# Optimization experiments

Measured on AMD Instinct MI355X. Metric: run time of the kernel, lower is better.

## Reference

```python
import jax, jax.numpy as jnp
import numpy as np

NUM_EXPERTS = 8
INPUT_SIZE = 2048
OUTPUT_SIZE = 8192
EXPERT_SIZES = np.array([3000, 5000, 4096, 2048, 6000, 4000, 4624, 4000], dtype=np.int64)  # sums to 32768
TOTAL_TOKENS = int(EXPERT_SIZES.sum())


def setup_inputs() -> dict:
    key = jax.random.key(0)
    k_in, k_w = jax.random.split(key)
    inputs = jax.random.normal(k_in, (TOTAL_TOKENS, INPUT_SIZE), dtype=jnp.float32)
    # per-expert Linear weights, torch layout [out, in]
    weights = jax.random.normal(k_w, (NUM_EXPERTS, OUTPUT_SIZE, INPUT_SIZE), dtype=jnp.float32) * 0.02
    expert_size = jnp.asarray(EXPERT_SIZES)
    return {"inputs": inputs, "weights": weights, "expert_size": expert_size}


def reference(inputs, weights, expert_size):
    # Grouped GEMM: split tokens by static per-expert counts, y_i = x_i @ W_i^T, concat.
    sizes = [int(s) for s in np.asarray(expert_size)]
    offsets = np.concatenate([[0], np.cumsum(sizes)])
    outs = []
    for i in range(len(sizes)):
        x_i = inputs[offsets[i]:offsets[i + 1]]  # [n_i, input_size]
        outs.append(jnp.einsum('ti,oi->to', x_i, weights[i]))  # [n_i, output_size]
    return jnp.concatenate(outs, axis=0)  # [total_tokens, output_size]
```

## Files before the change

### kernel.cpp

```cpp
#include <hip/hip_runtime.h>

typedef __bf16 bf16x8 __attribute__((ext_vector_type(8)));
typedef float  f32x4  __attribute__((ext_vector_type(4)));

#define KDIM 2048
#define NDIM 8192
#define MTOT 32768
#define BM 256
#define BN 256
#define BK 64
#define NT 32
#define NMT 131
#define NWG (NMT * 32)

__device__ __forceinline__ void gload_lds16(const void* g, void* l) {
    __builtin_amdgcn_global_load_lds(
        (const __attribute__((address_space(1))) void*)g,
        (__attribute__((address_space(3))) void*)l, 16, 0, 0);
}

__global__ __launch_bounds__(256) void convert_f32_bf16(
    const float* __restrict__ src, __bf16* __restrict__ dst, int n8)
{
    const int stride = gridDim.x * blockDim.x;
    for (int i = blockIdx.x * blockDim.x + threadIdx.x; i < n8; i += stride) {
        const f32x4* p = (const f32x4*)(src + (size_t)i * 8);
        f32x4 a = p[0], b = p[1];
        bf16x8 h;
        #pragma unroll
        for (int j = 0; j < 4; ++j) { h[j] = (__bf16)a[j]; h[4 + j] = (__bf16)b[j]; }
        *(bf16x8*)(dst + (size_t)i * 8) = h;
    }
}

__global__ void __launch_bounds__(512, 2) moe_gemm_4ph(
    const __bf16* __restrict__ A,
    const __bf16* __restrict__ W,
    float* __restrict__ C)
{
    __shared__ __bf16 As[2][BM * BK];
    __shared__ __bf16 Bs[2][BN * BK];

    const int tstart[9] = {0, 12, 32, 48, 56, 80, 96, 115, 131};
    const int offs[9]   = {0, 3000, 8000, 12096, 14144, 20144, 24144, 28768, 32768};

    const int bid = blockIdx.x;
    const int mt = bid >> 5;
    const int nt = bid & 31;

    int e = 0;
    #pragma unroll
    for (int i = 1; i < 8; ++i) e += (mt >= tstart[i]) ? 1 : 0;
    const int row0 = offs[e] + (mt - tstart[e]) * BM;
    int rows = offs[e + 1] - row0;
    if (rows > BM) rows = BM;
    const int col0 = nt * BN;

    const int tid  = threadIdx.x;
    const int lane = tid & 63;
    const int w    = tid >> 6;
    const int wm   = w >> 2;
    const int wn   = w & 3;

    const int lrow = lane >> 3;
    const int csrc = ((lane & 7) ^ lrow) * 8;

    const __bf16 *aX[2], *aY[2], *b0[2], *b1[2];
    int ldsAX[2], ldsAY[2], ldsB0[2], ldsB1[2];
    #pragma unroll
    for (int c = 0; c < 2; ++c) {
        const int q  = w * 2 + c;
        const int tX = q * 8 + (q & 8) * 8;
        const int tY = tX + 64;
        int rX = tX + lrow; rX = (rX < rows) ? rX : 0;
        int rY = tY + lrow; rY = (rY < rows) ? rY : 0;
        aX[c] = A + (size_t)(row0 + rX) * KDIM + csrc;
        aY[c] = A + (size_t)(row0 + rY) * KDIM + csrc;
        b0[c] = W + (size_t)(e * NDIM + col0 + q * 8 + lrow) * KDIM + csrc;
        b1[c] = W + (size_t)(e * NDIM + col0 + 128 + q * 8 + lrow) * KDIM + csrc;
        ldsAX[c] = tX * BK;
        ldsAY[c] = tY * BK;
        ldsB0[c] = (q * 8) * BK;
        ldsB1[c] = (128 + q * 8) * BK;
    }

#define STAGE_AX(p, o) { gload_lds16(aX[0] + (o), &As[p][ldsAX[0]]); \
                         gload_lds16(aX[1] + (o), &As[p][ldsAX[1]]); }
#define STAGE_AY(p, o) { gload_lds16(aY[0] + (o), &As[p][ldsAY[0]]); \
                         gload_lds16(aY[1] + (o), &As[p][ldsAY[1]]); }
#define STAGE_B0(p, o) { gload_lds16(b0[0] + (o), &Bs[p][ldsB0[0]]); \
                         gload_lds16(b0[1] + (o), &Bs[p][ldsB0[1]]); }
#define STAGE_B1(p, o) { gload_lds16(b1[0] + (o), &Bs[p][ldsB1[0]]); \
                         gload_lds16(b1[1] + (o), &Bs[p][ldsB1[1]]); }

    const int frow = lane & 15;
    const int g8   = (lane >> 4) * 8;
    const int swc  = (frow & 7) << 3;
    const int ck0  = g8 ^ swc;
    const int ck1  = (32 + g8) ^ swc;
    const int arow = wm * 128 + frow;
    const int brow = wn * 64 + frow;

    f32x4 acc[8][4];
    #pragma unroll
    for (int m = 0; m < 8; ++m)
        #pragma unroll
        for (int n = 0; n < 4; ++n)
            acc[m][n] = (f32x4){0.f, 0.f, 0.f, 0.f};

    bf16x8 bk0[4], bk1[4];

#define RD_B(p) { _Pragma("unroll") for (int n = 0; n < 4; ++n) { \
        bk0[n] = *(const bf16x8*)&Bs[p][(brow + n * 16) * BK + ck0]; \
        bk1[n] = *(const bf16x8*)&Bs[p][(brow + n * 16) * BK + ck1]; } }

#define MPHASE(p, h, STAGE, DOVM) { \
    bf16x8 av0[4], av1[4]; \
    _Pragma("unroll") for (int mm = 0; mm < 4; ++mm) { \
        av0[mm] = *(const bf16x8*)&As[p][(arow + (4 * (h) + mm) * 16) * BK + ck0]; \
        av1[mm] = *(const bf16x8*)&As[p][(arow + (4 * (h) + mm) * 16) * BK + ck1]; \
    } \
    STAGE; \
    if (DOVM) { asm volatile("s_waitcnt vmcnt(6)" ::: "memory"); } \
    __builtin_amdgcn_s_barrier(); \
    __builtin_amdgcn_s_setprio(1); \
    _Pragma("unroll") for (int mm = 0; mm < 4; ++mm) \
        _Pragma("unroll") for (int n = 0; n < 4; ++n) \
            acc[4 * (h) + mm][n] = __builtin_amdgcn_mfma_f32_16x16x32_bf16( \
                av0[mm], bk0[n], acc[4 * (h) + mm][n], 0, 0, 0); \
    _Pragma("unroll") for (int mm = 0; mm < 4; ++mm) \
        _Pragma("unroll") for (int n = 0; n < 4; ++n) \
            acc[4 * (h) + mm][n] = __builtin_amdgcn_mfma_f32_16x16x32_bf16( \
                av1[mm], bk1[n], acc[4 * (h) + mm][n], 0, 0, 0); \
    __builtin_amdgcn_s_setprio(0); }

    STAGE_AX(0, 0); STAGE_AY(0, 0); STAGE_B0(0, 0); STAGE_B1(0, 0);
    STAGE_B0(1, BK); STAGE_B1(1, BK); STAGE_AX(1, BK);
    asm volatile("s_waitcnt vmcnt(6)" ::: "memory");
    __builtin_amdgcn_s_barrier();

    #pragma unroll 1
    for (int i = 0; i < 16; ++i) {
        const int t1o = (2 * i + 1) * BK;
        int s2 = 2 * i + 2; if (s2 > NT - 1) s2 = NT - 1;
        int s3 = 2 * i + 3; if (s3 > NT - 1) s3 = NT - 1;
        const int s2o = s2 * BK;
        const int s3o = s3 * BK;

        RD_B(0);
        MPHASE(0, 0, { STAGE_AY(1, t1o); }, 0);
        MPHASE(0, 1, { STAGE_B0(0, s2o); STAGE_B1(0, s2o); STAGE_AX(0, s2o); }, 1);

        RD_B(1);
        MPHASE(1, 0, { STAGE_AY(0, s2o); }, 0);
        MPHASE(1, 1, { STAGE_B0(1, s3o); STAGE_B1(1, s3o); STAGE_AX(1, s3o); }, 1);
    }

    const int crow = (lane >> 4) * 4;
    const int ccol = lane & 15;
    #pragma unroll
    for (int m = 0; m < 8; ++m) {
        #pragma unroll
        for (int j2 = 0; j2 < 4; ++j2) {
            const int r = wm * 128 + m * 16 + crow + j2;
            if (r < rows) {
                float* dst = C + (size_t)(row0 + r) * NDIM + col0 + wn * 64 + ccol;
                #pragma unroll
                for (int n = 0; n < 4; ++n)
                    dst[n * 16] = acc[m][n][j2];
            }
        }
    }
#undef STAGE_AX
#undef STAGE_AY
#undef STAGE_B0
#undef STAGE_B1
#undef RD_B
#undef MPHASE
}

__global__ __launch_bounds__(256) void moe_gemm_f32(
    const float* __restrict__ A, const float* __restrict__ W, float* __restrict__ C)
{
    __shared__ __bf16 Asb[128][64];
    __shared__ __bf16 Bsb[128][64];

    const int tstart[9] = {0, 24, 64, 96, 112, 159, 191, 228, 260};
    const int offs[9]   = {0, 3000, 8000, 12096, 14144, 20144, 24144, 28768, 32768};

    const int mt = blockIdx.y;
    int e = 0;
    #pragma unroll
    for (int i = 1; i < 8; ++i) e += (mt >= tstart[i]) ? 1 : 0;
    const int row0 = offs[e] + (mt - tstart[e]) * 128;
    int rows = offs[e + 1] - row0;
    if (rows > 128) rows = 128;
    const int col0 = blockIdx.x * 128;

    const float* __restrict__ Abase = A + (size_t)row0 * KDIM;
    const float* __restrict__ Wbase = W + ((size_t)e * NDIM + (size_t)col0) * KDIM;

    const int tid  = threadIdx.x;
    const int lane = tid & 63;
    const int wid  = tid >> 6;
    const int wr   = (wid >> 1) * 64;
    const int wc   = (wid & 1) * 64;
    const int srow = tid >> 2;
    const int scol = (tid & 3) * 16;

    f32x4 acc[4][4];
    #pragma unroll
    for (int m = 0; m < 4; ++m)
        #pragma unroll
        for (int n = 0; n < 4; ++n)
            acc[m][n] = (f32x4){0.f, 0.f, 0.f, 0.f};
    const f32x4 fzero = (f32x4){0.f, 0.f, 0.f, 0.f};

    for (int k0 = 0; k0 < KDIM; k0 += 64) {
        __syncthreads();
        #pragma unroll
        for (int rr = 0; rr < 2; ++rr) {
            const int r = srow + rr * 64;
            {
                const bool valid = (r < rows);
                const float* pa = Abase + (size_t)r * KDIM + k0 + scol;
                f32x4 v[4];
                #pragma unroll
                for (int i = 0; i < 4; ++i) v[i] = valid ? *(const f32x4*)(pa + 4 * i) : fzero;
                bf16x8 h0, h1;
                #pragma unroll
                for (int i = 0; i < 8; ++i) {
                    h0[i] = (__bf16)v[i >> 2][i & 3];
                    h1[i] = (__bf16)v[2 + (i >> 2)][i & 3];
                }
                *((bf16x8*)&Asb[r][scol]) = h0;
                *((bf16x8*)&Asb[r][scol + 8]) = h1;
            }
            {
                const float* pb = Wbase + (size_t)r * KDIM + k0 + scol;
                f32x4 v[4];
                #pragma unroll
                for (int i = 0; i < 4; ++i) v[i] = *(const f32x4*)(pb + 4 * i);
                bf16x8 h0, h1;
                #pragma unroll
                for (int i = 0; i < 8; ++i) {
                    h0[i] = (__bf16)v[i >> 2][i & 3];
                    h1[i] = (__bf16)v[2 + (i >> 2)][i & 3];
                }
                *((bf16x8*)&Bsb[r][scol]) = h0;
                *((bf16x8*)&Bsb[r][scol + 8]) = h1;
            }
        }
        __syncthreads();
        #pragma unroll
        for (int ks = 0; ks < 2; ++ks) {
            const int kb = ks * 32 + (lane >> 4) * 8;
            bf16x8 af[4], bfr[4];
            #pragma unroll
            for (int m = 0; m < 4; ++m)
                af[m] = *((const bf16x8*)&Asb[wr + m * 16 + (lane & 15)][kb]);
            #pragma unroll
            for (int n = 0; n < 4; ++n)
                bfr[n] = *((const bf16x8*)&Bsb[wc + n * 16 + (lane & 15)][kb]);
            #pragma unroll
            for (int m = 0; m < 4; ++m)
                #pragma unroll
                for (int n = 0; n < 4; ++n)
                    acc[m][n] = __builtin_amdgcn_mfma_f32_16x16x32_bf16(
                        af[m], bfr[n], acc[m][n], 0, 0, 0);
        }
    }

    const int crow = (lane >> 4) * 4;
    const int ccol = lane & 15;
    #pragma unroll
    for (int m = 0; m < 4; ++m) {
        #pragma unroll
        for (int j = 0; j < 4; ++j) {
            const int r = wr + m * 16 + crow + j;
            if (r < rows) {
                float* dst = C + (size_t)(row0 + r) * NDIM + col0 + wc + ccol;
                #pragma unroll
                for (int n = 0; n < 4; ++n)
                    dst[n * 16] = acc[m][n][j];
            }
        }
    }
}

extern "C" void kernel_launch(void* const* d_in, const int* in_sizes, int n_in,
                              void* d_out, int out_size, void* d_ws, size_t ws_size,
                              hipStream_t stream) {
    const float* A = (const float*)d_in[0];
    const float* W = (const float*)d_in[1];
    float* C = (float*)d_out;

    const size_t nA = (size_t)MTOT * KDIM;
    const size_t nW = (size_t)8 * NDIM * KDIM;
    const size_t WS_NEED = (nA + nW) * 2;

    if (ws_size >= WS_NEED) {
        __bf16* Abf = (__bf16*)d_ws;
        __bf16* Wbf = (__bf16*)((char*)d_ws + nA * 2);
        hipLaunchKernelGGL(convert_f32_bf16, dim3(2048), dim3(256), 0, stream,
                           A, Abf, (int)(nA / 8));
        hipLaunchKernelGGL(convert_f32_bf16, dim3(2048), dim3(256), 0, stream,
                           W, Wbf, (int)(nW / 8));
        hipLaunchKernelGGL(moe_gemm_4ph, dim3(NWG), dim3(512), 0, stream,
                           Abf, Wbf, C);
    } else {
        hipLaunchKernelGGL(moe_gemm_f32, dim3(NDIM / 128, 260), dim3(256), 0, stream,
                           A, W, C);
    }
}
```

Before: 1.266 ms.

## Double-buffer LDS-to-register fragments so reads overlap the previous MFMA cluster

Restructures the main loop so each phase issues its global staging and barrier first, then loads the next A/B fragments from LDS into a second register set before running the MFMA cluster on the already-loaded set. sched_barrier fences keep the compiler from interleaving the two. The aim is to hide LDS read latency behind matrix-core work. In exchange it doubles fragment register usage, which risks spills or pressure at the 512-thread, 2-block launch bound. It also changes barrier placement relative to buffer overwrites, which could open hazards.

```diff
diff --git a/kernel.cpp b/kernel.cpp
--- a/kernel.cpp
+++ b/kernel.cpp
@@ -33,7 +33,7 @@
     }
 }
 
-__global__ void __launch_bounds__(512, 2) moe_gemm_4ph(
+__global__ void __launch_bounds__(512, 2) moe_gemm_rdb(
     const __bf16* __restrict__ A,
     const __bf16* __restrict__ W,
     float* __restrict__ C)
@@ -108,36 +108,38 @@
         for (int n = 0; n < 4; ++n)
             acc[m][n] = (f32x4){0.f, 0.f, 0.f, 0.f};
 
-    bf16x8 bk0[4], bk1[4];
-
-#define RD_B(p) { _Pragma("unroll") for (int n = 0; n < 4; ++n) { \
-        bk0[n] = *(const bf16x8*)&Bs[p][(brow + n * 16) * BK + ck0]; \
-        bk1[n] = *(const bf16x8*)&Bs[p][(brow + n * 16) * BK + ck1]; } }
-
-#define MPHASE(p, h, STAGE, DOVM) { \
-    bf16x8 av0[4], av1[4]; \
-    _Pragma("unroll") for (int mm = 0; mm < 4; ++mm) { \
-        av0[mm] = *(const bf16x8*)&As[p][(arow + (4 * (h) + mm) * 16) * BK + ck0]; \
-        av1[mm] = *(const bf16x8*)&As[p][(arow + (4 * (h) + mm) * 16) * BK + ck1]; \
-    } \
-    STAGE; \
-    if (DOVM) { asm volatile("s_waitcnt vmcnt(6)" ::: "memory"); } \
-    __builtin_amdgcn_s_barrier(); \
+    bf16x8 bkA0[4], bkA1[4], bkB0[4], bkB1[4];
+    bf16x8 aA0[4], aA1[4], aB0[4], aB1[4];
+
+#define RD_BSET(d0, d1, p) { _Pragma("unroll") for (int n = 0; n < 4; ++n) { \
+        d0[n] = *(const bf16x8*)&Bs[p][(brow + n * 16) * BK + ck0]; \
+        d1[n] = *(const bf16x8*)&Bs[p][(brow + n * 16) * BK + ck1]; } }
+
+#define RD_ASET(d0, d1, p, h) { _Pragma("unroll") for (int mm = 0; mm < 4; ++mm) { \
+        d0[mm] = *(const bf16x8*)&As[p][(arow + (4 * (h) + mm) * 16) * BK + ck0]; \
+        d1[mm] = *(const bf16x8*)&As[p][(arow + (4 * (h) + mm) * 16) * BK + ck1]; } }
+
+#define MFMA_CL(h, a0, a1, bq0, bq1) { \
     __builtin_amdgcn_s_setprio(1); \
     _Pragma("unroll") for (int mm = 0; mm < 4; ++mm) \
         _Pragma("unroll") for (int n = 0; n < 4; ++n) \
             acc[4 * (h) + mm][n] = __builtin_amdgcn_mfma_f32_16x16x32_bf16( \
-                av0[mm], bk0[n], acc[4 * (h) + mm][n], 0, 0, 0); \
+                a0[mm], bq0[n], acc[4 * (h) + mm][n], 0, 0, 0); \
     _Pragma("unroll") for (int mm = 0; mm < 4; ++mm) \
         _Pragma("unroll") for (int n = 0; n < 4; ++n) \
             acc[4 * (h) + mm][n] = __builtin_amdgcn_mfma_f32_16x16x32_bf16( \
-                av1[mm], bk1[n], acc[4 * (h) + mm][n], 0, 0, 0); \
+                a1[mm], bq1[n], acc[4 * (h) + mm][n], 0, 0, 0); \
     __builtin_amdgcn_s_setprio(0); }
+
+#define FENCE asm volatile("" ::: "memory")
 
     STAGE_AX(0, 0); STAGE_AY(0, 0); STAGE_B0(0, 0); STAGE_B1(0, 0);
     STAGE_B0(1, BK); STAGE_B1(1, BK); STAGE_AX(1, BK);
     asm volatile("s_waitcnt vmcnt(6)" ::: "memory");
     __builtin_amdgcn_s_barrier();
+    FENCE;
+    RD_BSET(bkA0, bkA1, 0);
+    RD_ASET(aA0, aA1, 0, 0);
 
     #pragma unroll 1
     for (int i = 0; i < 16; ++i) {
@@ -147,13 +149,37 @@
         const int s2o = s2 * BK;
         const int s3o = s3 * BK;
 
-        RD_B(0);
-        MPHASE(0, 0, { STAGE_AY(1, t1o); }, 0);
-        MPHASE(0, 1, { STAGE_B0(0, s2o); STAGE_B1(0, s2o); STAGE_AX(0, s2o); }, 1);
-
-        RD_B(1);
-        MPHASE(1, 0, { STAGE_AY(0, s2o); }, 0);
-        MPHASE(1, 1, { STAGE_B0(1, s3o); STAGE_B1(1, s3o); STAGE_AX(1, s3o); }, 1);
+        STAGE_AY(1, t1o);
+        __builtin_amdgcn_s_barrier();
+        FENCE;
+        RD_ASET(aB0, aB1, 0, 1);
+        __builtin_amdgcn_sched_barrier(0);
+        MFMA_CL(0, aA0, aA1, bkA0, bkA1);
+
+        STAGE_B0(0, s2o); STAGE_B1(0, s2o); STAGE_AX(0, s2o);
+        asm volatile("s_waitcnt vmcnt(6)" ::: "memory");
+        __builtin_amdgcn_s_barrier();
+        FENCE;
+        RD_BSET(bkB0, bkB1, 1);
+        RD_ASET(aA0, aA1, 1, 0);
+        __builtin_amdgcn_sched_barrier(0);
+        MFMA_CL(1, aB0, aB1, bkA0, bkA1);
+
+        STAGE_AY(0, s2o);
+        __builtin_amdgcn_s_barrier();
+        FENCE;
+        RD_ASET(aB0, aB1, 1, 1);
+        __builtin_amdgcn_sched_barrier(0);
+        MFMA_CL(0, aA0, aA1, bkB0, bkB1);
+
+        STAGE_B0(1, s3o); STAGE_B1(1, s3o); STAGE_AX(1, s3o);
+        asm volatile("s_waitcnt vmcnt(6)" ::: "memory");
+        __builtin_amdgcn_s_barrier();
+        FENCE;
+        RD_BSET(bkA0, bkA1, 0);
+        RD_ASET(aA0, aA1, 0, 0);
+        __builtin_amdgcn_sched_barrier(0);
+        MFMA_CL(1, aB0, aB1, bkB0, bkB1);
     }
 
     const int crow = (lane >> 4) * 4;
@@ -175,8 +201,10 @@
 #undef STAGE_AY
 #undef STAGE_B0
 #undef STAGE_B1
-#undef RD_B
-#undef MPHASE
+#undef RD_BSET
+#undef RD_ASET
+#undef MFMA_CL
+#undef FENCE
 }
 
 __global__ __launch_bounds__(256) void moe_gemm_f32(
@@ -306,7 +334,7 @@
                            A, Abf, (int)(nA / 8));
         hipLaunchKernelGGL(convert_f32_bf16, dim3(2048), dim3(256), 0, stream,
                            W, Wbf, (int)(nW / 8));
-        hipLaunchKernelGGL(moe_gemm_4ph, dim3(NWG), dim3(512), 0, stream,
+        hipLaunchKernelGGL(moe_gemm_rdb, dim3(NWG), dim3(512), 0, stream,
                            Abf, Wbf, C);
     } else {
         hipLaunchKernelGGL(moe_gemm_f32, dim3(NDIM / 128, 260), dim3(256), 0, stream,
```

Result: slower. 3.681 ms (+190.7%).

## Triple-buffer A tiles in LDS and restructure GEMM pipeline phases

Applied to the files above, without the earlier changes.

Replaces the two-stage A/B LDS ring with three A buffers and two B buffers. Each K-tile's A operand is now staged in one four-load group instead of being split into halves across phases. The main loop is rewritten as four phases with explicit LDS reads, prefetch issue, MFMA clusters, and vmcnt(8) waits. The intent is to prefetch A further ahead and hide global-to-LDS latency better behind the matrix math. The cost is LDS use rising to 160KB per workgroup, the full capacity, and the vmcnt accounting must still match the new issue order.

```diff
diff --git a/kernel.cpp b/kernel.cpp
--- a/kernel.cpp
+++ b/kernel.cpp
@@ -12,6 +12,8 @@
 #define NT 32
 #define NMT 131
 #define NWG (NMT * 32)
+#define ABUF (BM * BK)
+#define BBUF (BN * BK)
 
 __device__ __forceinline__ void gload_lds16(const void* g, void* l) {
     __builtin_amdgcn_global_load_lds(
@@ -33,13 +35,13 @@
     }
 }
 
-__global__ void __launch_bounds__(512, 2) moe_gemm_4ph(
+__global__ void __launch_bounds__(512, 2) moe_gemm_3a(
     const __bf16* __restrict__ A,
     const __bf16* __restrict__ W,
     float* __restrict__ C)
 {
-    __shared__ __bf16 As[2][BM * BK];
-    __shared__ __bf16 Bs[2][BN * BK];
+    __shared__ __bf16 AsF[3 * ABUF];
+    __shared__ __bf16 BsF[2 * BBUF];
 
     const int tstart[9] = {0, 12, 32, 48, 56, 80, 96, 115, 131};
     const int offs[9]   = {0, 3000, 8000, 12096, 14144, 20144, 24144, 28768, 32768};
@@ -84,14 +86,16 @@
         ldsB1[c] = (128 + q * 8) * BK;
     }
 
-#define STAGE_AX(p, o) { gload_lds16(aX[0] + (o), &As[p][ldsAX[0]]); \
-                         gload_lds16(aX[1] + (o), &As[p][ldsAX[1]]); }
-#define STAGE_AY(p, o) { gload_lds16(aY[0] + (o), &As[p][ldsAY[0]]); \
-                         gload_lds16(aY[1] + (o), &As[p][ldsAY[1]]); }
-#define STAGE_B0(p, o) { gload_lds16(b0[0] + (o), &Bs[p][ldsB0[0]]); \
-                         gload_lds16(b0[1] + (o), &Bs[p][ldsB0[1]]); }
-#define STAGE_B1(p, o) { gload_lds16(b1[0] + (o), &Bs[p][ldsB1[0]]); \
-                         gload_lds16(b1[1] + (o), &Bs[p][ldsB1[1]]); }
+#define STAGE_A(ab, o) { \
+    gload_lds16(aX[0] + (o), &AsF[(ab) * ABUF + ldsAX[0]]); \
+    gload_lds16(aX[1] + (o), &AsF[(ab) * ABUF + ldsAX[1]]); \
+    gload_lds16(aY[0] + (o), &AsF[(ab) * ABUF + ldsAY[0]]); \
+    gload_lds16(aY[1] + (o), &AsF[(ab) * ABUF + ldsAY[1]]); }
+#define STAGE_B(bb, o) { \
+    gload_lds16(b0[0] + (o), &BsF[(bb) * BBUF + ldsB0[0]]); \
+    gload_lds16(b0[1] + (o), &BsF[(bb) * BBUF + ldsB0[1]]); \
+    gload_lds16(b1[0] + (o), &BsF[(bb) * BBUF + ldsB1[0]]); \
+    gload_lds16(b1[1] + (o), &BsF[(bb) * BBUF + ldsB1[1]]); }
 
     const int frow = lane & 15;
     const int g8   = (lane >> 4) * 8;
@@ -109,20 +113,17 @@
             acc[m][n] = (f32x4){0.f, 0.f, 0.f, 0.f};
 
     bf16x8 bk0[4], bk1[4];
-
-#define RD_B(p) { _Pragma("unroll") for (int n = 0; n < 4; ++n) { \
-        bk0[n] = *(const bf16x8*)&Bs[p][(brow + n * 16) * BK + ck0]; \
-        bk1[n] = *(const bf16x8*)&Bs[p][(brow + n * 16) * BK + ck1]; } }
-
-#define MPHASE(p, h, STAGE, DOVM) { \
-    bf16x8 av0[4], av1[4]; \
-    _Pragma("unroll") for (int mm = 0; mm < 4; ++mm) { \
-        av0[mm] = *(const bf16x8*)&As[p][(arow + (4 * (h) + mm) * 16) * BK + ck0]; \
-        av1[mm] = *(const bf16x8*)&As[p][(arow + (4 * (h) + mm) * 16) * BK + ck1]; \
-    } \
-    STAGE; \
-    if (DOVM) { asm volatile("s_waitcnt vmcnt(6)" ::: "memory"); } \
-    __builtin_amdgcn_s_barrier(); \
+    bf16x8 av0[4], av1[4];
+
+#define RD_B(bb) { _Pragma("unroll") for (int n = 0; n < 4; ++n) { \
+        bk0[n] = *(const bf16x8*)&BsF[(bb) * BBUF + (brow + n * 16) * BK + ck0]; \
+        bk1[n] = *(const bf16x8*)&BsF[(bb) * BBUF + (brow + n * 16) * BK + ck1]; } }
+
+#define RD_A(ab, h) { _Pragma("unroll") for (int mm = 0; mm < 4; ++mm) { \
+        av0[mm] = *(const bf16x8*)&AsF[(ab) * ABUF + (arow + (4 * (h) + mm) * 16) * BK + ck0]; \
+        av1[mm] = *(const bf16x8*)&AsF[(ab) * ABUF + (arow + (4 * (h) + mm) * 16) * BK + ck1]; } }
+
+#define MFMA_CL(h) { \
     __builtin_amdgcn_s_setprio(1); \
     _Pragma("unroll") for (int mm = 0; mm < 4; ++mm) \
         _Pragma("unroll") for (int n = 0; n < 4; ++n) \
@@ -134,26 +135,52 @@
                 av1[mm], bk1[n], acc[4 * (h) + mm][n], 0, 0, 0); \
     __builtin_amdgcn_s_setprio(0); }
 
-    STAGE_AX(0, 0); STAGE_AY(0, 0); STAGE_B0(0, 0); STAGE_B1(0, 0);
-    STAGE_B0(1, BK); STAGE_B1(1, BK); STAGE_AX(1, BK);
-    asm volatile("s_waitcnt vmcnt(6)" ::: "memory");
+#define FENCE asm volatile("" ::: "memory")
+
+    STAGE_A(0, 0); STAGE_B(0, 0);
+    STAGE_A(1, BK); STAGE_B(1, BK);
+    asm volatile("s_waitcnt vmcnt(8)" ::: "memory");
     __builtin_amdgcn_s_barrier();
 
+    int a0 = 0;
     #pragma unroll 1
     for (int i = 0; i < 16; ++i) {
-        const int t1o = (2 * i + 1) * BK;
-        int s2 = 2 * i + 2; if (s2 > NT - 1) s2 = NT - 1;
-        int s3 = 2 * i + 3; if (s3 > NT - 1) s3 = NT - 1;
-        const int s2o = s2 * BK;
-        const int s3o = s3 * BK;
-
+        int a1 = a0 + 1; if (a1 >= 3) a1 -= 3;
+        int a2 = a0 + 2; if (a2 >= 3) a2 -= 3;
+        int t2 = 2 * i + 2; if (t2 > NT - 1) t2 = NT - 1;
+        int t3 = 2 * i + 3; if (t3 > NT - 1) t3 = NT - 1;
+        const int t2o = t2 * BK;
+        const int t3o = t3 * BK;
+
+        FENCE;
         RD_B(0);
-        MPHASE(0, 0, { STAGE_AY(1, t1o); }, 0);
-        MPHASE(0, 1, { STAGE_B0(0, s2o); STAGE_B1(0, s2o); STAGE_AX(0, s2o); }, 1);
-
+        RD_A(a0, 0);
+        STAGE_A(a2, t2o);
+        MFMA_CL(0);
+        __builtin_amdgcn_s_barrier();
+
+        FENCE;
+        RD_A(a0, 1);
+        STAGE_B(0, t2o);
+        MFMA_CL(1);
+        asm volatile("s_waitcnt vmcnt(8)" ::: "memory");
+        __builtin_amdgcn_s_barrier();
+
+        FENCE;
         RD_B(1);
-        MPHASE(1, 0, { STAGE_AY(0, s2o); }, 0);
-        MPHASE(1, 1, { STAGE_B0(1, s3o); STAGE_B1(1, s3o); STAGE_AX(1, s3o); }, 1);
+        RD_A(a1, 0);
+        STAGE_A(a0, t3o);
+        MFMA_CL(0);
+        __builtin_amdgcn_s_barrier();
+
+        FENCE;
+        RD_A(a1, 1);
+        STAGE_B(1, t3o);
+        MFMA_CL(1);
+        asm volatile("s_waitcnt vmcnt(8)" ::: "memory");
+        __builtin_amdgcn_s_barrier();
+
+        a0 = a2;
     }
 
     const int crow = (lane >> 4) * 4;
@@ -171,12 +198,12 @@
             }
         }
     }
-#undef STAGE_AX
-#undef STAGE_AY
-#undef STAGE_B0
-#undef STAGE_B1
+#undef STAGE_A
+#undef STAGE_B
 #undef RD_B
-#undef MPHASE
+#undef RD_A
+#undef MFMA_CL
+#undef FENCE
 }
 
 __global__ __launch_bounds__(256) void moe_gemm_f32(
@@ -306,7 +333,7 @@
                            A, Abf, (int)(nA / 8));
         hipLaunchKernelGGL(convert_f32_bf16, dim3(2048), dim3(256), 0, stream,
                            W, Wbf, (int)(nW / 8));
-        hipLaunchKernelGGL(moe_gemm_4ph, dim3(NWG), dim3(512), 0, stream,
+        hipLaunchKernelGGL(moe_gemm_3a, dim3(NWG), dim3(512), 0, stream,
                            Abf, Wbf, C);
     } else {
         hipLaunchKernelGGL(moe_gemm_f32, dim3(NDIM / 128, 260), dim3(256), 0, stream,
```

New measurement: 1.430 ms. +12.9%, slower.
